# Optimization experiments

Measured on AMD Instinct MI355X. Metric: run time of the kernel, lower is better.

Reference implementation:

```python
import jax, jax.numpy as jnp
import numpy as np

B, DIM, OC, H, W, HEADS = 4, 128, 128, 128, 128, 8
L = H * W
_BN_INV = 1.0 / (1.0 + 1e-5) ** 0.5  # eval-mode BN: running_mean=0, running_var=1


def conv2d(x, w, b=None, groups=1, pad=0):
    y = jax.lax.conv_general_dilated(
        x, w, (1, 1), [(pad, pad), (pad, pad)],
        dimension_numbers=('NCHW', 'OIHW', 'NCHW'),
        feature_group_count=groups)
    if b is not None:
        y = y + b[None, :, None, None]
    return y


def bn(x, g, b):
    return x * (g * _BN_INV)[None, :, None, None] + b[None, :, None, None]


def ln(x, g, b, eps=1e-5):
    m = jnp.mean(x, -1, keepdims=True)
    v = jnp.mean((x - m) ** 2, -1, keepdims=True)
    return (x - m) * jax.lax.rsqrt(v + eps) * g + b


def rope_tables(h, w, c, base=10000.0):
    k_max = c // 4
    theta = 1.0 / base ** (np.arange(k_max, dtype=np.float32) / k_max)
    gi, gj = np.meshgrid(np.arange(h, dtype=np.float32),
                         np.arange(w, dtype=np.float32), indexing='ij')
    ang = np.concatenate([gi[..., None] * theta, gj[..., None] * theta], -1)  # (h,w,c//2)
    return jnp.asarray(np.cos(ang)), jnp.asarray(np.sin(ang))


def apply_rope(x, cs, sn):  # x: (b,h,w,c); consecutive pairs = (re, im)
    xr, xi = x[..., 0::2], x[..., 1::2]
    return jnp.stack([cs * xr - sn * xi, sn * xr + cs * xi], -1).reshape(x.shape)


def linear_attn(x, qk_w, qk_b, lepe_w, lepe_b, h, w):
    b, n, c = x.shape
    hd = c // HEADS
    qk = x @ qk_w.T + qk_b
    q = jax.nn.elu(qk[..., :c]) + 1.0
    k = jax.nn.elu(qk[..., c:]) + 1.0
    cs, sn = rope_tables(h, w, c)

    def heads(t):  # (b,n,c) -> (b,HEADS,n,hd)
        return t.reshape(b, n, HEADS, hd).transpose(0, 2, 1, 3)

    q_r = heads(apply_rope(q.reshape(b, h, w, c), cs, sn).reshape(b, n, c))
    k_r = heads(apply_rope(k.reshape(b, h, w, c), cs, sn).reshape(b, n, c))
    qh, kh, vh = heads(q), heads(k), heads(x)
    k_mean = jnp.mean(kh, axis=2, keepdims=True)                      # (b,Hd,1,hd)
    z = 1.0 / (jnp.einsum('bhnd,bhmd->bhnm', qh, k_mean) + 1e-6)      # (b,Hd,n,1)
    s = n ** -0.5
    kv = jnp.einsum('bhnd,bhne->bhde', k_r * s, vh * s)               # (b,Hd,hd,hd)
    out = jnp.einsum('bhnd,bhde->bhne', q_r, kv) * z
    out = out.transpose(0, 2, 1, 3).reshape(b, n, c)
    v_img = x.reshape(b, h, w, c).transpose(0, 3, 1, 2)
    lepe = conv2d(v_img, lepe_w, lepe_b, groups=c, pad=1)
    return out + lepe.transpose(0, 2, 3, 1).reshape(b, n, c)


def fmt_block(xb, fw1, fb1, f_g, f_be, fw2, fb2, n_g, n_be):
    t = jnp.fft.fft2(xb)                                              # (B,C,H,W) complex
    wgt = jax.nn.relu(bn(conv2d(t.real, fw1, fb1), f_g, f_be))
    wgt = jax.nn.sigmoid(conv2d(wgt, fw2, fb2))
    f = jnp.abs(jnp.fft.ifft2(wgt * t))
    f = jax.nn.relu(bn(f, n_g, n_be))
    return f.reshape(f.shape[0], f.shape[1], -1).transpose(0, 2, 1)   # (B,L,C)


def _forward(x, c1_w, c1_b, c1_g, c1_be, cpe1_w, cpe1_b,
             fw1, fb1, f_g, f_be, fw2, fb2, nbn_g, nbn_be,
             ln1_g, ln1_b, d3w1, d3b1, d3w2, d5w1, d5b1, d5w2,
             ap_w, ap_b, ip2_w, ip2_b, dwc2_w, dwc2_b,
             qk_w, qk_b, lepe_w, lepe_b, op_w, op_b,
             cpe2_w, cpe2_b, ln2_g, ln2_b,
             ffn_w1, ffn_b1, ffn_w2, ffn_b2, po_w,
             red_w, red_b, red_g, red_be):
    Bb, C, Hh, Ww = x.shape
    Ll = Hh * Ww
    to_img = lambda t: t.reshape(Bb, Hh, Ww, C).transpose(0, 3, 1, 2)   # (B,L,C)->(B,C,H,W)
    to_seq = lambda t: t.transpose(0, 2, 3, 1).reshape(Bb, Ll, -1)       # (B,C,H,W)->(B,L,C)

    x_0 = jax.nn.relu(bn(conv2d(x, c1_w, c1_b), c1_g, c1_be))           # (B,OC,H,W)
    xt = to_seq(x + conv2d(x, cpe1_w, cpe1_b, groups=C, pad=1))
    shortcut = xt
    fmt1 = fmt_block(to_img(xt), fw1, fb1, f_g, f_be, fw2, fb2, nbn_g, nbn_be)

    x_s = ln(xt, ln1_g, ln1_b)
    xs_img = to_img(x_s)
    x_s3 = conv2d(conv2d(xs_img, d3w1, d3b1), d3w2, None, groups=C // 2, pad=1)
    x_s5 = conv2d(conv2d(xs_img, d5w1, d5b1), d5w2, None, groups=C // 2, pad=2)
    act_res = jax.nn.silu(to_seq(conv2d(xs_img, ap_w, ap_b)))

    def branch(t):  # (B,C/2,H,W) -> (B,L,C/2)
        t = conv2d(t, ip2_w, ip2_b)
        t = jax.nn.silu(conv2d(t, dwc2_w, dwc2_b, groups=C // 2, pad=1))
        return to_seq(t)

    a3 = linear_attn(branch(x_s3), qk_w, qk_b, lepe_w, lepe_b, Hh, Ww)
    a5 = linear_attn(branch(x_s5), qk_w, qk_b, lepe_w, lepe_b, Hh, Ww)
    xs = jnp.concatenate([a3, a5], -1)
    xs = to_seq(conv2d(to_img(xs * act_res), op_w, op_b))

    xt = shortcut + xs + fmt1
    xt = xt + to_seq(conv2d(to_img(xt), cpe2_w, cpe2_b, groups=C, pad=1))
    fmt2 = fmt_block(to_img(xt), fw1, fb1, f_g, f_be, fw2, fb2, nbn_g, nbn_be)
    h2 = ln(xt, ln2_g, ln2_b)
    ffn = jax.nn.gelu(h2 @ ffn_w1.T + ffn_b1, approximate=False) @ ffn_w2.T + ffn_b2
    xt = xt + ffn + fmt2

    xo = conv2d(to_img(xt), po_w)                                        # (B,OC,H,W)
    cat = jnp.concatenate([x_0, xo], 1)
    return jax.nn.relu(bn(conv2d(cat, red_w, red_b), red_g, red_be)) + x_0


def setup_inputs():
    key = jax.random.key(0)
    it = iter(jax.random.split(key, 64))

    def w(shape, s=0.05):
        return jax.random.normal(next(it), shape, jnp.float32) * s

    d, oc = DIM, OC
    ones = lambda n: jnp.ones((n,), jnp.float32)
    zeros = lambda n: jnp.zeros((n,), jnp.float32)
    return {
        'x': jax.random.normal(next(it), (B, d, H, W), jnp.float32),
        'c1_w': w((oc, d, 1, 1)), 'c1_b': w((oc,), 0.01), 'c1_g': ones(oc), 'c1_be': zeros(oc),
        'cpe1_w': w((d, 1, 3, 3)), 'cpe1_b': w((d,), 0.01),
        'fw1': w((d // 16, d, 1, 1)), 'fb1': w((d // 16,), 0.01),
        'f_g': ones(d // 16), 'f_be': zeros(d // 16),
        'fw2': w((d, d // 16, 1, 1)), 'fb2': w((d,), 0.01),
        'nbn_g': ones(d), 'nbn_be': zeros(d),
        'ln1_g': ones(d), 'ln1_b': zeros(d),
        'd3w1': w((d, d, 1, 1)), 'd3b1': w((d,), 0.01), 'd3w2': w((d // 2, 2, 3, 3)),
        'd5w1': w((d, d, 1, 1)), 'd5b1': w((d,), 0.01), 'd5w2': w((d // 2, 2, 5, 5)),
        'ap_w': w((d, d, 1, 1)), 'ap_b': w((d,), 0.01),
        'ip2_w': w((d // 2, d // 2, 1, 1)), 'ip2_b': w((d // 2,), 0.01),
        'dwc2_w': w((d // 2, 1, 3, 3)), 'dwc2_b': w((d // 2,), 0.01),
        'qk_w': w((d, d // 2)), 'qk_b': w((d,), 0.01),
        'lepe_w': w((d // 2, 1, 3, 3)), 'lepe_b': w((d // 2,), 0.01),
        'op_w': w((d, d, 1, 1)), 'op_b': w((d,), 0.01),
        'cpe2_w': w((d, 1, 3, 3)), 'cpe2_b': w((d,), 0.01),
        'ln2_g': ones(d), 'ln2_b': zeros(d),
        'ffn_w1': w((4, d)), 'ffn_b1': w((4,), 0.01),
        'ffn_w2': w((d, 4)), 'ffn_b2': w((d,), 0.01),
        'po_w': w((oc, d, 1, 1)),
        'red_w': w((oc, 2 * oc, 1, 1)), 'red_b': w((oc,), 0.01),
        'red_g': ones(oc), 'red_be': zeros(oc),
    }


def reference(x, c1_w, c1_b, c1_g, c1_be, cpe1_w, cpe1_b,
              fw1, fb1, f_g, f_be, fw2, fb2, nbn_g, nbn_be,
              ln1_g, ln1_b, d3w1, d3b1, d3w2, d5w1, d5b1, d5w2,
              ap_w, ap_b, ip2_w, ip2_b, dwc2_w, dwc2_b,
              qk_w, qk_b, lepe_w, lepe_b, op_w, op_b,
              cpe2_w, cpe2_b, ln2_g, ln2_b,
              ffn_w1, ffn_b1, ffn_w2, ffn_b2, po_w,
              red_w, red_b, red_g, red_be):
    return _forward(x, c1_w, c1_b, c1_g, c1_be, cpe1_w, cpe1_b,
                    fw1, fb1, f_g, f_be, fw2, fb2, nbn_g, nbn_be,
                    ln1_g, ln1_b, d3w1, d3b1, d3w2, d5w1, d5b1, d5w2,
                    ap_w, ap_b, ip2_w, ip2_b, dwc2_w, dwc2_b,
                    qk_w, qk_b, lepe_w, lepe_b, op_w, op_b,
                    cpe2_w, cpe2_b, ln2_g, ln2_b,
                    ffn_w1, ffn_b1, ffn_w2, ffn_b2, po_w,
                    red_w, red_b, red_g, red_be)
```

## Files before the change

kernel.cpp:

```cpp
#include <hip/hip_runtime.h>
#include <math.h>

typedef unsigned short bf16_t;
typedef __attribute__((ext_vector_type(8))) short short8;
typedef __attribute__((ext_vector_type(4))) float f32x4;

#define B_ 4
#define C_ 128
#define H_ 128
#define W_ 128
#define L_ (H_*W_)
#define NS  ((size_t)B_*L_*C_)
#define NH  ((size_t)B_*L_*64)
#define NSP ((size_t)L_*C_)
#define PI_F 3.14159265358979323846f
#define BN_INV 0.9999950000374997f
#define THETA_SC 0.8304820237218406f
#define TOTW 157148
#define W16SHIFT 107548

__device__ __forceinline__ float ldf(bf16_t v){ return __uint_as_float(((unsigned)v)<<16); }
__device__ __forceinline__ bf16_t f2b(float f){
  unsigned u = __float_as_uint(f);
  u += 0x7fffu + ((u>>16)&1u);
  return (bf16_t)(u>>16);
}

#define WGSZ ((size_t)B_*8*L_)
#define ACCSZ 2304
#define CWSZ 157184
#define CW16SZF 78592
#define WSF (6*NS + 3*NH + WGSZ + ACCSZ + CWSZ + CW16SZF + 16)
__device__ float g_ws[WSF];

__global__ void k_probe(const bf16_t* __restrict__ xb, int* __restrict__ flag){
  __shared__ int vote;
  if (threadIdx.x == 0) vote = 0;
  __syncthreads();
  int bad = 0;
  for (int i = threadIdx.x; i < 2048; i += 256) {
    float v = ldf(xb[2*i]);
    if (!(fabsf(v) < 1e6f)) bad = 1;
  }
  if (bad) atomicOr(&vote, 1);
  __syncthreads();
  if (threadIdx.x == 0) *flag = vote;
}

struct P47 { const void* p[47]; };
__device__ __constant__ int c_wsz[47] = {
  16384,128,128,128,1152,128,1024,8,8,8,1024,128,128,128,128,128,
  16384,128,1152,16384,128,3200,16384,128,4096,64,576,64,8192,128,
  576,64,16384,128,1152,128,128,128,512,4,512,128,16384,32768,128,128,128};

__global__ __launch_bounds__(256) void k_cvt(P47 ps, const int* __restrict__ flagp,
                                             float* __restrict__ dst){
  int g = blockIdx.x*256 + threadIdx.x;
  if (g >= TOTW) return;
  int fl = *flagp;
  int idx = 0, off = g;
  while (off >= c_wsz[idx]) { off -= c_wsz[idx]; idx++; }
  const void* s = ps.p[idx];
  dst[g] = fl ? ((const float*)s)[off] : ldf(((const bf16_t*)s)[off]);
}

__global__ __launch_bounds__(256) void k_cvt16(const float* __restrict__ src, bf16_t* __restrict__ dst){
  int g = blockIdx.x*256 + threadIdx.x;
  if (g >= TOTW) return;
  dst[g + (g >= W16SHIFT ? 4 : 0)] = f2b(src[g]);
}

__global__ void k_zero(float* p, int n){
  int i = blockIdx.x*256 + threadIdx.x;
  if (i < n) p[i] = 0.f;
}

__device__ __forceinline__ void tw_fwd(int lane, float* tc, float* ts) {
  sincosf(-PI_F * (float)lane * (1.f/64.f), &ts[0], &tc[0]);
  int i = 1;
  #pragma unroll
  for (int m = 32; m >= 1; m >>= 1, i++) {
    int k = lane & (m-1);
    sincosf(-PI_F * (float)k / (float)m, &ts[i], &tc[i]);
  }
}
__device__ __forceinline__ void tw_inv(int lane, float* tc, float* ts) {
  int i = 0;
  #pragma unroll
  for (int m = 1; m <= 32; m <<= 1, i++) {
    int k = lane & (m-1);
    sincosf(PI_F * (float)k / (float)m, &ts[i], &tc[i]);
  }
  sincosf(PI_F * (float)lane * (1.f/64.f), &ts[6], &tc[6]);
}

__device__ __forceinline__ void fft128_fwd(float& lor, float& loi, float& hir, float& hii,
                                           int lane, const float* tc, const float* ts) {
  {
    float s = ts[0], c = tc[0];
    float ar = lor, ai = loi;
    float dr = ar - hir, di = ai - hii;
    lor = ar + hir; loi = ai + hii;
    hir = dr*c - di*s; hii = dr*s + di*c;
  }
  int i = 1;
  #pragma unroll
  for (int m = 32; m >= 1; m >>= 1, i++) {
    float s = ts[i], c = tc[i];
    bool up = (lane & m) != 0;
    {
      float orr = __shfl_xor(lor, m), oii = __shfl_xor(loi, m);
      float sr = lor + orr, si = loi + oii;
      float dr = orr - lor, di = oii - loi;
      float tr = dr*c - di*s, ti = dr*s + di*c;
      lor = up ? tr : sr; loi = up ? ti : si;
    }
    {
      float orr = __shfl_xor(hir, m), oii = __shfl_xor(hii, m);
      float sr = hir + orr, si = hii + oii;
      float dr = orr - hir, di = oii - hii;
      float tr = dr*c - di*s, ti = dr*s + di*c;
      hir = up ? tr : sr; hii = up ? ti : si;
    }
  }
}

__device__ __forceinline__ void fft128_inv(float& lor, float& loi, float& hir, float& hii,
                                           int lane, const float* tc, const float* ts) {
  int i = 0;
  #pragma unroll
  for (int m = 1; m <= 32; m <<= 1, i++) {
    float s = ts[i], c = tc[i];
    bool up = (lane & m) != 0;
    {
      float orr = __shfl_xor(lor, m), oii = __shfl_xor(loi, m);
      float qr = orr*c - oii*s, qi = orr*s + oii*c;
      float lo_r = lor + qr, lo_i = loi + qi;
      float mr = lor*c - loi*s, mi = lor*s + loi*c;
      float up_r = orr - mr, up_i = oii - mi;
      lor = up ? up_r : lo_r; loi = up ? up_i : lo_i;
    }
    {
      float orr = __shfl_xor(hir, m), oii = __shfl_xor(hii, m);
      float qr = orr*c - oii*s, qi = orr*s + oii*c;
      float lo_r = hir + qr, lo_i = hii + qi;
      float mr = hir*c - hii*s, mi = hir*s + hii*c;
      float up_r = orr - mr, up_i = oii - mi;
      hir = up ? up_r : lo_r; hii = up ? up_i : lo_i;
    }
  }
  {
    float s = ts[6], c = tc[6];
    float qr = hir*c - hii*s, qi = hir*s + hii*c;
    float pr = lor, pi = loi;
    lor = pr + qr; loi = pi + qi;
    hir = pr - qr; hii = pi - qi;
  }
}

__global__ __launch_bounds__(256) void k_fft_row_fwd_seq(
    const float* __restrict__ in, float* __restrict__ re, float* __restrict__ im) {
  __shared__ float T[64*130];
  int tid = threadIdx.x;
  int bid = blockIdx.x;
  int ch = (bid & 1) * 64;
  int h  = (bid >> 1) & 127;
  int b  = bid >> 8;
  const float* ip = in + ((size_t)b*L_ + (size_t)h*128)*128 + ch;
  #pragma unroll
  for (int it = 0; it < 8; it++) {
    int idx = it*256 + tid;
    int c4 = (idx & 15)*4, w = idx >> 4;
    float4 v = *(const float4*)(ip + (size_t)w*128 + c4);
    T[(c4+0)*130 + w] = v.x;
    T[(c4+1)*130 + w] = v.y;
    T[(c4+2)*130 + w] = v.z;
    T[(c4+3)*130 + w] = v.w;
  }
  __syncthreads();
  int lane = tid & 63, wv = tid >> 6;
  float tc[7], ts[7];
  tw_fwd(lane, tc, ts);
  size_t obase = (size_t)(b*128 + ch)*L_ + (size_t)h*128;
  for (int i = 0; i < 16; i++) {
    int cc = wv*16 + i;
    float lor = T[cc*130 + lane], loi = 0.f;
    float hir = T[cc*130 + 64 + lane], hii = 0.f;
    fft128_fwd(lor, loi, hir, hii, lane, tc, ts);
    size_t o = obase + (size_t)cc*L_;
    re[o + lane] = lor;      im[o + lane] = loi;
    re[o + lane + 64] = hir; im[o + lane + 64] = hii;
  }
}

__global__ __launch_bounds__(256) void k_fft_col_fwd(float* __restrict__ re, float* __restrict__ im) {
  __shared__ float Lre[128][33];
  __shared__ float Lim[128][33];
  int tid = threadIdx.x;
  size_t img = blockIdx.x >> 2;
  int w0 = (blockIdx.x & 3) * 32;
  float* rp = re + img * (size_t)L_ + w0;
  float* ip = im + img * (size_t)L_ + w0;
  for (int i = tid; i < 4096; i += 256) {
    int h = i >> 5, wl = i & 31;
    Lre[h][wl] = rp[(size_t)h*W_ + wl];
    Lim[h][wl] = ip[(size_t)h*W_ + wl];
  }
  __syncthreads();
  int lane = tid & 63, wv = tid >> 6;
  float tc[7], ts[7];
  tw_fwd(lane, tc, ts);
  for (int i = 0; i < 8; i++) {
    int col = wv*8 + i;
    float lor = Lre[lane][col], loi = Lim[lane][col];
    float hir = Lre[lane+64][col], hii = Lim[lane+64][col];
    fft128_fwd(lor, loi, hir, hii, lane, tc, ts);
    Lre[lane][col]=lor; Lim[lane][col]=loi;
    Lre[lane+64][col]=hir; Lim[lane+64][col]=hii;
  }
  __syncthreads();
  for (int i = tid; i < 4096; i += 256) {
    int h = i >> 5, wl = i & 31;
    rp[(size_t)h*W_ + wl] = Lre[h][wl];
    ip[(size_t)h*W_ + wl] = Lim[h][wl];
  }
}

__global__ __launch_bounds__(256) void k_fft_col_inv_scaled(
    float* __restrict__ re, float* __restrict__ im,
    const float* __restrict__ wg1, const float* __restrict__ fw2,
    const float* __restrict__ fb2) {
  __shared__ float Lre[128][33];
  __shared__ float Lim[128][33];
  __shared__ float w2r[8];
  int tid = threadIdx.x;
  size_t img = blockIdx.x >> 2;
  int c = (int)(img & 127);
  int b = (int)(img >> 7);
  int w0 = (blockIdx.x & 3) * 32;
  if (tid < 8) w2r[tid] = fw2[c*8 + tid];
  float b2 = fb2[c];
  float* rp = re + img * (size_t)L_ + w0;
  float* ip = im + img * (size_t)L_ + w0;
  const float* wgp = wg1 + (size_t)b*8*L_ + w0;
  __syncthreads();
  for (int i = tid; i < 4096; i += 256) {
    int h = i >> 5, wl = i & 31;
    size_t p = (size_t)h*W_ + wl;
    float a = b2;
    #pragma unroll
    for (int o = 0; o < 8; o++) a += w2r[o] * wgp[(size_t)o*L_ + p];
    float wgt = 1.f/(1.f+expf(-a));
    Lre[h][wl] = rp[p] * wgt;
    Lim[h][wl] = ip[p] * wgt;
  }
  __syncthreads();
  int lane = tid & 63, wv = tid >> 6;
  float tc[7], ts[7];
  tw_inv(lane, tc, ts);
  for (int i = 0; i < 8; i++) {
    int col = wv*8 + i;
    float lor = Lre[lane][col], loi = Lim[lane][col];
    float hir = Lre[lane+64][col], hii = Lim[lane+64][col];
    fft128_inv(lor, loi, hir, hii, lane, tc, ts);
    Lre[lane][col]=lor*(1.f/128.f); Lim[lane][col]=loi*(1.f/128.f);
    Lre[lane+64][col]=hir*(1.f/128.f); Lim[lane+64][col]=hii*(1.f/128.f);
  }
  __syncthreads();
  for (int i = tid; i < 4096; i += 256) {
    int h = i >> 5, wl = i & 31;
    rp[(size_t)h*W_ + wl] = Lre[h][wl];
    ip[(size_t)h*W_ + wl] = Lim[h][wl];
  }
}

__global__ __launch_bounds__(256) void k_fft_row_inv_abs_seq(
    const float* __restrict__ re, const float* __restrict__ im,
    const float* __restrict__ ng, const float* __restrict__ nbe,
    const float* __restrict__ add1, const float* __restrict__ add2,
    float* __restrict__ out) {
  __shared__ float T[64*130];
  int tid = threadIdx.x;
  int bid = blockIdx.x;
  int ch = (bid & 1) * 64;
  int h  = (bid >> 1) & 127;
  int b  = bid >> 8;
  int lane = tid & 63, wv = tid >> 6;
  float tc[7], ts[7];
  tw_inv(lane, tc, ts);
  size_t ibase = (size_t)(b*128 + ch)*L_ + (size_t)h*128;
  for (int i = 0; i < 16; i++) {
    int cc = wv*16 + i;
    size_t o = ibase + (size_t)cc*L_;
    float lor = re[o + lane], loi = im[o + lane];
    float hir = re[o + lane + 64], hii = im[o + lane + 64];
    fft128_inv(lor, loi, hir, hii, lane, tc, ts);
    float sg = ng[ch+cc]*BN_INV, sb = nbe[ch+cc];
    T[cc*130 + lane]      = fmaxf(sqrtf(lor*lor+loi*loi)*(1.f/128.f)*sg + sb, 0.f);
    T[cc*130 + 64 + lane] = fmaxf(sqrtf(hir*hir+hii*hii)*(1.f/128.f)*sg + sb, 0.f);
  }
  __syncthreads();
  size_t sb0 = ((size_t)b*L_ + (size_t)h*128)*128 + ch;
  #pragma unroll
  for (int it = 0; it < 8; it++) {
    int idx = it*256 + tid;
    int c4 = (idx & 15)*4, w = idx >> 4;
    size_t off = sb0 + (size_t)w*128 + c4;
    float4 v;
    v.x = T[(c4+0)*130 + w];
    v.y = T[(c4+1)*130 + w];
    v.z = T[(c4+2)*130 + w];
    v.w = T[(c4+3)*130 + w];
    float4 x1 = *(const float4*)(add1 + off);
    float4 x2 = *(const float4*)(add2 + off);
    v.x += x1.x + x2.x; v.y += x1.y + x2.y;
    v.z += x1.z + x2.z; v.w += x1.w + x2.w;
    *(float4*)(out + off) = v;
  }
}

__global__ __launch_bounds__(256) void k_freq1(const float* __restrict__ tre,
    const float* __restrict__ fw1, const float* __restrict__ fb1,
    const float* __restrict__ fg, const float* __restrict__ fbe,
    float* __restrict__ wg1) {
  __shared__ float w1s[1024];
  int tid = threadIdx.x;
  for (int i = tid; i < 1024; i += 256) w1s[i] = fw1[i];
  __syncthreads();
  size_t g = (size_t)blockIdx.x*256 + tid;
  int p = (int)(g & (L_-1));
  int b = (int)(g >> 14);
  const float* tp = tre + (size_t)b*128*L_ + p;
  float acc[8];
  #pragma unroll
  for (int o = 0; o < 8; o++) acc[o] = 0.f;
  for (int c = 0; c < 128; c++) {
    float v = tp[(size_t)c*L_];
    #pragma unroll
    for (int o = 0; o < 8; o++) acc[o] += w1s[o*128+c]*v;
  }
  size_t ob = (size_t)b*8*L_ + p;
  #pragma unroll
  for (int o = 0; o < 8; o++) {
    float v = (acc[o] + fb1[o]) * (fg[o]*BN_INV) + fbe[o];
    wg1[ob + (size_t)o*L_] = fmaxf(v, 0.f);
  }
}

template<bool DUAL>
__global__ void k_p2s(const void* __restrict__ src, float* __restrict__ dst,
                      const float* __restrict__ add1, const float* __restrict__ add2,
                      const int* __restrict__ flagp) {
  __shared__ float tile[32][33];
  int fl = DUAL ? *flagp : 1;
  int b = blockIdx.z;
  int p0 = blockIdx.x*32, c0 = blockIdx.y*32;
  int tx = threadIdx.x, ty = threadIdx.y;
  size_t base_in = (size_t)b*NSP;
  #pragma unroll
  for (int k = 0; k < 4; k++) {
    size_t off = base_in + (size_t)(c0+ty+8*k)*L_ + p0 + tx;
    float v;
    if (DUAL && !fl) v = ldf(((const bf16_t*)src)[off]);
    else             v = ((const float*)src)[off];
    tile[ty+8*k][tx] = v;
  }
  __syncthreads();
  size_t base = (size_t)b*NSP;
  #pragma unroll
  for (int k = 0; k < 4; k++) {
    size_t idx = base + (size_t)(p0+ty+8*k)*C_ + c0 + tx;
    float v = tile[tx][ty+8*k];
    if (add1) v += add1[idx];
    if (add2) v += add2[idx];
    dst[idx] = v;
  }
}

template<int CC, int MODE>
__global__ __launch_bounds__(256) void k_dw3(const float* __restrict__ in,
    const float* __restrict__ w, const float* __restrict__ bias,
    float* __restrict__ out) {
  __shared__ float wl[9*CC];
  int tid = threadIdx.x;
  for (int i = tid; i < 9*CC; i += 256) {
    int tap = i / CC, ch = i % CC;
    wl[i] = w[ch*9 + tap];
  }
  __syncthreads();
  size_t g = (size_t)blockIdx.x*256 + tid;
  int c = (int)(g & (CC-1));
  float wr[9];
  #pragma unroll
  for (int t = 0; t < 9; t++) wr[t] = wl[t*CC + c];
  size_t s = g / CC;
  int w0 = (int)(s & 31) * 4;
  int hp = (int)((s >> 5) & 127);
  int b  = (int)(s >> 12);
  const float* ip = in + (size_t)b*L_*CC + c;
  float bi = bias[c];
  float a0 = bi, a1 = bi, a2 = bi, a3 = bi;
  #pragma unroll
  for (int dh = -1; dh <= 1; dh++) {
    int h2 = hp + dh;
    if ((unsigned)h2 >= 128u) continue;
    const float* rp = ip + (size_t)h2*W_*CC;
    float px[6];
    #pragma unroll
    for (int x = 0; x < 6; x++) {
      int w2 = w0 - 1 + x;
      px[x] = ((unsigned)w2 < 128u) ? rp[(size_t)w2*CC] : 0.f;
    }
    #pragma unroll
    for (int dw = 0; dw < 3; dw++) {
      float f = wr[(dh+1)*3 + dw];
      a0 += f*px[dw];   a1 += f*px[dw+1];
      a2 += f*px[dw+2]; a3 += f*px[dw+3];
    }
  }
  size_t tb = (size_t)b*L_ + (size_t)hp*W_ + w0;
  if (MODE == 0) {
    out[(tb+0)*CC + c] = in[(tb+0)*CC + c] + a0;
    out[(tb+1)*CC + c] = in[(tb+1)*CC + c] + a1;
    out[(tb+2)*CC + c] = in[(tb+2)*CC + c] + a2;
    out[(tb+3)*CC + c] = in[(tb+3)*CC + c] + a3;
  } else {
    out[(tb+0)*CC + c] = a0 / (1.f + expf(-a0));
    out[(tb+1)*CC + c] = a1 / (1.f + expf(-a1));
    out[(tb+2)*CC + c] = a2 / (1.f + expf(-a2));
    out[(tb+3)*CC + c] = a3 / (1.f + expf(-a3));
  }
}

template<int K>
__global__ __launch_bounds__(256) void k_gconv(const float* __restrict__ in,
    const float* __restrict__ w, float* __restrict__ out) {
  __shared__ float wl[K*K*128];
  int tid = threadIdx.x;
  for (int i = tid; i < 128*K*K; i += 256) {
    int tap = i >> 7, ch = i & 127;
    wl[i] = w[ch*(K*K) + tap];
  }
  __syncthreads();
  size_t g = (size_t)blockIdx.x*256 + tid;
  int oc = (int)(g & 63);
  float wx[K*K], wy[K*K];
  #pragma unroll
  for (int t = 0; t < K*K; t++) {
    wx[t] = wl[t*128 + 2*oc];
    wy[t] = wl[t*128 + 2*oc + 1];
  }
  size_t s = g >> 6;
  int w0 = (int)(s & 31) * 4;
  int hp = (int)((s >> 5) & 127);
  int b  = (int)(s >> 12);
  const float* ip = in + (size_t)b*L_*128 + 2*oc;
  constexpr int P = K/2;
  float a0 = 0.f, a1 = 0.f, a2 = 0.f, a3 = 0.f;
  #pragma unroll
  for (int kh = 0; kh < K; kh++) {
    int h2 = hp + kh - P;
    if ((unsigned)h2 >= 128u) continue;
    const float* rp = ip + (size_t)h2*W_*128;
    float2 px[K+3];
    #pragma unroll
    for (int x = 0; x < K+3; x++) {
      int w2 = w0 - P + x;
      px[x] = ((unsigned)w2 < 128u) ? *(const float2*)(rp + (size_t)w2*128)
                                    : make_float2(0.f, 0.f);
    }
    #pragma unroll
    for (int kw = 0; kw < K; kw++) {
      float fx = wx[kh*K + kw], fy = wy[kh*K + kw];
      a0 += fx*px[kw+0].x + fy*px[kw+0].y;
      a1 += fx*px[kw+1].x + fy*px[kw+1].y;
      a2 += fx*px[kw+2].x + fy*px[kw+2].y;
      a3 += fx*px[kw+3].x + fy*px[kw+3].y;
    }
  }
  size_t tb = (size_t)b*L_ + (size_t)hp*W_ + w0;
  out[(tb+0)*64 + oc] = a0;
  out[(tb+1)*64 + oc] = a1;
  out[(tb+2)*64 + oc] = a2;
  out[(tb+3)*64 + oc] = a3;
}

template<int CIN, int COUT, int EPI, bool MUL>
__global__ __launch_bounds__(256) void k_mfma_tok(
    const float* __restrict__ in, const float* __restrict__ mulp,
    const bf16_t* __restrict__ W16, const float* __restrict__ bias,
    float* __restrict__ out) {
  constexpr int NO = COUT/16;
  int tid = threadIdx.x;
  int lane = tid & 63, wv = tid >> 6;
  int m = lane & 15, q = lane >> 4;
  size_t t0 = (size_t)blockIdx.x*64 + (size_t)wv*16;
  f32x4 acc[NO];
  #pragma unroll
  for (int i = 0; i < NO; i++) acc[i] = (f32x4){0.f,0.f,0.f,0.f};
  for (int k0 = 0; k0 < CIN; k0 += 32) {
    const float* ap = in + (t0 + m)*CIN + k0 + q*8;
    float4 a0 = *(const float4*)ap;
    float4 a1 = *(const float4*)(ap + 4);
    if (MUL) {
      const float* mp = mulp + (t0 + m)*CIN + k0 + q*8;
      float4 m0 = *(const float4*)mp;
      float4 m1 = *(const float4*)(mp + 4);
      a0.x*=m0.x; a0.y*=m0.y; a0.z*=m0.z; a0.w*=m0.w;
      a1.x*=m1.x; a1.y*=m1.y; a1.z*=m1.z; a1.w*=m1.w;
    }
    union { short s[8]; short8 v; } af;
    af.s[0]=(short)f2b(a0.x); af.s[1]=(short)f2b(a0.y);
    af.s[2]=(short)f2b(a0.z); af.s[3]=(short)f2b(a0.w);
    af.s[4]=(short)f2b(a1.x); af.s[5]=(short)f2b(a1.y);
    af.s[6]=(short)f2b(a1.z); af.s[7]=(short)f2b(a1.w);
    #pragma unroll
    for (int o = 0; o < NO; o++) {
      short8 bf = *(const short8*)(W16 + (size_t)(o*16 + m)*CIN + k0 + q*8);
      acc[o] = __builtin_amdgcn_mfma_f32_16x16x32_bf16(af.v, bf, acc[o], 0, 0, 0);
    }
  }
  #pragma unroll
  for (int o = 0; o < NO; o++) {
    float bv = (EPI >= 1) ? bias[o*16 + m] : 0.f;
    #pragma unroll
    for (int r = 0; r < 4; r++) {
      int row = q*4 + r;
      float v = acc[o][r] + bv;
      if (EPI == 2) v = v / (1.f + expf(-v));
      if (EPI == 3) v = v > 0.f ? v + 1.f : expf(v);
      out[(t0 + row)*COUT + o*16 + m] = v;
    }
  }
}

template<int CIN, bool DUALOUT, bool ADDX>
__global__ __launch_bounds__(256) void k_mfma_pout(
    const float* __restrict__ in1, const float* __restrict__ in2,
    const bf16_t* __restrict__ W16, const float* __restrict__ bias,
    const float* __restrict__ gam, const float* __restrict__ bet,
    const float* __restrict__ addp, void* __restrict__ out,
    const int* __restrict__ flagp) {
  constexpr int NO = 8;
  int fl = DUALOUT ? *flagp : 1;
  int tid = threadIdx.x;
  int lane = tid & 63, wv = tid >> 6;
  int m = lane & 15, q = lane >> 4;
  size_t t0 = (size_t)blockIdx.x*64 + (size_t)wv*16;
  f32x4 acc[NO];
  #pragma unroll
  for (int i = 0; i < NO; i++) acc[i] = (f32x4){0.f,0.f,0.f,0.f};
  for (int k0 = 0; k0 < CIN; k0 += 32) {
    const float* src = (CIN == 128 || k0 < 128)
        ? (in1 + (t0 + m)*128 + k0)
        : (in2 + (t0 + m)*128 + (k0 - 128));
    float4 a0 = *(const float4*)(src + q*8);
    float4 a1 = *(const float4*)(src + q*8 + 4);
    union { short s[8]; short8 v; } af;
    af.s[0]=(short)f2b(a0.x); af.s[1]=(short)f2b(a0.y);
    af.s[2]=(short)f2b(a0.z); af.s[3]=(short)f2b(a0.w);
    af.s[4]=(short)f2b(a1.x); af.s[5]=(short)f2b(a1.y);
    af.s[6]=(short)f2b(a1.z); af.s[7]=(short)f2b(a1.w);
    #pragma unroll
    for (int o = 0; o < NO; o++) {
      short8 bf = *(const short8*)(W16 + (size_t)(o*16 + m)*CIN + k0 + q*8);
      acc[o] = __builtin_amdgcn_mfma_f32_16x16x32_bf16(af.v, bf, acc[o], 0, 0, 0);
    }
  }
  int b = (int)(t0 >> 14);
  int p0 = (int)(t0 & (L_-1)) + q*4;
  #pragma unroll
  for (int ot = 0; ot < NO; ot++) {
    int o = ot*16 + m;
    float bi = bias[o], gm = gam[o]*BN_INV, be = bet[o];
    size_t idx = ((size_t)b*128 + o)*L_ + p0;
    float4 r4;
    float* rr = (float*)&r4;
    #pragma unroll
    for (int r = 0; r < 4; r++) {
      float v = acc[ot][r] + bi;
      v = fmaxf(v*gm + be, 0.f);
      rr[r] = v;
    }
    if (ADDX) {
      float4 av = *(const float4*)(addp + idx);
      r4.x += av.x; r4.y += av.y; r4.z += av.z; r4.w += av.w;
    }
    if (DUALOUT && !fl) {
      ushort4 s4;
      s4.x = f2b(r4.x); s4.y = f2b(r4.y); s4.z = f2b(r4.z); s4.w = f2b(r4.w);
      *(ushort4*)((bf16_t*)out + idx) = s4;
    } else {
      *(float4*)((float*)out + idx) = r4;
    }
  }
}

__global__ __launch_bounds__(256) void k_ln(const float* __restrict__ in,
    const float* __restrict__ g, const float* __restrict__ be, float* __restrict__ out) {
  int tid = threadIdx.x, lane = tid & 63;
  size_t t = (size_t)blockIdx.x*4 + (tid >> 6);
  const float* row = in + t*128;
  float2 v = *(const float2*)(row + lane*2);
  float s = v.x + v.y, ss = v.x*v.x + v.y*v.y;
  #pragma unroll
  for (int m = 1; m < 64; m <<= 1) { s += __shfl_xor(s, m); ss += __shfl_xor(ss, m); }
  float mean = s*(1.f/128.f);
  float inv = rsqrtf(ss*(1.f/128.f) - mean*mean + 1e-5f);
  float2 o;
  o.x = (v.x-mean)*inv*g[lane*2]   + be[lane*2];
  o.y = (v.y-mean)*inv*g[lane*2+1] + be[lane*2+1];
  *(float2*)(out + t*128 + lane*2) = o;
}

__global__ __launch_bounds__(256) void k_ln_ffn(const float* __restrict__ in,
    const float* __restrict__ g, const float* __restrict__ be,
    const float* __restrict__ w1, const float* __restrict__ b1,
    const float* __restrict__ w2, const float* __restrict__ b2,
    float* __restrict__ out) {
  int tid = threadIdx.x, lane = tid & 63;
  size_t t = (size_t)blockIdx.x*4 + (tid >> 6);
  const float* row = in + t*128;
  float2 v = *(const float2*)(row + lane*2);
  float s = v.x + v.y, ss = v.x*v.x + v.y*v.y;
  #pragma unroll
  for (int m = 1; m < 64; m <<= 1) { s += __shfl_xor(s, m); ss += __shfl_xor(ss, m); }
  float mean = s*(1.f/128.f);
  float inv = rsqrtf(ss*(1.f/128.f) - mean*mean + 1e-5f);
  float hx = (v.x-mean)*inv*g[lane*2]   + be[lane*2];
  float hy = (v.y-mean)*inv*g[lane*2+1] + be[lane*2+1];
  float hp0 = hx*w1[0*128+lane*2] + hy*w1[0*128+lane*2+1];
  float hp1 = hx*w1[1*128+lane*2] + hy*w1[1*128+lane*2+1];
  float hp2 = hx*w1[2*128+lane*2] + hy*w1[2*128+lane*2+1];
  float hp3 = hx*w1[3*128+lane*2] + hy*w1[3*128+lane*2+1];
  #pragma unroll
  for (int m = 1; m < 64; m <<= 1) {
    hp0 += __shfl_xor(hp0, m); hp1 += __shfl_xor(hp1, m);
    hp2 += __shfl_xor(hp2, m); hp3 += __shfl_xor(hp3, m);
  }
  float hv0, hv1, hv2, hv3;
  { float a = hp0 + b1[0]; hv0 = 0.5f*a*(1.f+erff(a*0.7071067811865476f)); }
  { float a = hp1 + b1[1]; hv1 = 0.5f*a*(1.f+erff(a*0.7071067811865476f)); }
  { float a = hp2 + b1[2]; hv2 = 0.5f*a*(1.f+erff(a*0.7071067811865476f)); }
  { float a = hp3 + b1[3]; hv3 = 0.5f*a*(1.f+erff(a*0.7071067811865476f)); }
  int cx = lane*2, cy = lane*2+1;
  float2 o;
  o.x = hv0*w2[cx*4+0] + hv1*w2[cx*4+1] + hv2*w2[cx*4+2] + hv3*w2[cx*4+3] + b2[cx];
  o.y = hv0*w2[cy*4+0] + hv1*w2[cy*4+1] + hv2*w2[cy*4+2] + hv3*w2[cy*4+3] + b2[cy];
  *(float2*)(out + t*128 + lane*2) = o;
}

__global__ __launch_bounds__(256) void k_kv(
    const float* __restrict__ qk, const float* __restrict__ v,
    float* __restrict__ akv_g, float* __restrict__ aks_g) {
  __shared__ float kvred[512];
  __shared__ float ksred[64];
  int tid = threadIdx.x;
  for (int i = tid; i < 512; i += 256) kvred[i] = 0.f;
  if (tid < 64) ksred[tid] = 0.f;
  __syncthreads();
  int lane = tid & 63, wv = tid >> 6;
  size_t t0 = (size_t)blockIdx.x * 64;
  int b = (int)(t0 >> 14);
  int pr = lane >> 1;
  float theta = exp2f(-(float)(pr & 15) * THETA_SC);
  bool use_i = pr < 16;
  int hbase = lane & 56;
  float akv[8];
  #pragma unroll
  for (int d = 0; d < 8; d++) akv[d] = 0.f;
  float aks = 0.f;
  for (int it = 0; it < 16; it++) {
    size_t t = t0 + (size_t)wv*16 + it;
    float k = qk[t*128 + 64 + lane];
    float xv = v[t*64 + lane];
    int l = (int)(t & (L_-1));
    float pos = use_i ? (float)(l >> 7) : (float)(l & 127);
    float sn, cs; sincosf(pos*theta, &sn, &cs);
    float kp = __shfl_xor(k, 1);
    float kr = (lane & 1) ? (sn*kp + cs*k) : (cs*k - sn*kp);
    #pragma unroll
    for (int d = 0; d < 8; d++) {
      float krd = __shfl(kr, hbase + d);
      akv[d] += krd * xv;
    }
    aks += k;
  }
  int h8 = lane >> 3, e = lane & 7;
  #pragma unroll
  for (int d = 0; d < 8; d++)
    atomicAdd(&kvred[h8*64 + d*8 + e], akv[d]);
  atomicAdd(&ksred[lane], aks);
  __syncthreads();
  for (int i = tid; i < 512; i += 256) atomicAdd(&akv_g[b*512 + i], kvred[i]);
  if (tid < 64) atomicAdd(&aks_g[b*64 + tid], ksred[tid]);
}

__global__ __launch_bounds__(256) void k_attn2(
    const float* __restrict__ qk, const float* __restrict__ x,
    const float* __restrict__ akv_g, const float* __restrict__ aks_g,
    const float* __restrict__ lw, const float* __restrict__ lb,
    float* __restrict__ out, int coff) {
  __shared__ float kv[512];
  __shared__ float km[64];
  __shared__ float lwl[576];
  int tid = threadIdx.x;
  size_t t0 = (size_t)blockIdx.x * 32;
  int b = (int)(t0 >> 14);
  const float invn = 1.f/16384.f;
  for (int i = tid; i < 512; i += 256) kv[i] = akv_g[b*512 + i]*invn;
  if (tid < 64) km[tid] = aks_g[b*64 + tid]*invn;
  for (int i = tid; i < 576; i += 256) lwl[i] = lw[i];
  __syncthreads();
  int lane = tid & 63, wv = tid >> 6;
  int pr = lane >> 1;
  float theta = exp2f(-(float)(pr & 15) * THETA_SC);
  bool use_i = pr < 16;
  int hbase = lane & 56, e = lane & 7;
  float lbv = lb[lane];
  const float* xb = x + ((size_t)b << 14) * 64;
  for (int it = 0; it < 8; it++) {
    size_t t = t0 + (size_t)wv*8 + it;
    int l = (int)(t & (L_-1));
    int ipos = l >> 7, jpos = l & 127;
    float q = qk[t*128 + lane];
    float p = q * km[lane];
    p += __shfl_xor(p, 1); p += __shfl_xor(p, 2); p += __shfl_xor(p, 4);
    float z = 1.f/(p + 1e-6f);
    float pos = use_i ? (float)ipos : (float)jpos;
    float sn, cs; sincosf(pos*theta, &sn, &cs);
    float qp = __shfl_xor(q, 1);
    float qr = (lane & 1) ? (sn*qp + cs*q) : (cs*q - sn*qp);
    float acc = 0.f;
    #pragma unroll
    for (int d = 0; d < 8; d++) {
      float qrd = __shfl(qr, hbase + d);
      acc += qrd * kv[hbase*8 + d*8 + e];
    }
    acc *= z;
    float lp = lbv;
    #pragma unroll
    for (int dh = -1; dh <= 1; dh++) {
      int h2 = ipos + dh; if ((unsigned)h2 >= 128u) continue;
      #pragma unroll
      for (int dw = -1; dw <= 1; dw++) {
        int w2 = jpos + dw; if ((unsigned)w2 >= 128u) continue;
        lp += lwl[lane*9 + (dh+1)*3 + (dw+1)] * xb[((size_t)(h2 << 7) + w2)*64 + lane];
      }
    }
    out[t*128 + coff + lane] = acc + lp;
  }
}

extern "C" void kernel_launch(void* const* d_in, const int* in_sizes, int n_in,
                              void* d_out, int out_size, void* d_ws, size_t ws_size,
                              hipStream_t stream) {
  (void)in_sizes; (void)n_in; (void)out_size;

  float* base;
  if (ws_size >= WSF * sizeof(float)) {
    base = (float*)d_ws;
  } else {
    void* p = nullptr;
    hipGetSymbolAddress(&p, HIP_SYMBOL(g_ws));
    base = (float*)p;
  }
  float* P0 = base;
  float* PA = base + 1*NS;
  float* PB = base + 2*NS;
  float* PC = base + 3*NS;
  float* PD = base + 4*NS;
  float* PF = base + 5*NS;
  float* H0 = base + 6*NS;
  float* H1 = H0 + NH;
  float* H2 = H1 + NH;
  float* WG = H2 + NH;
  float* ACC = WG + WGSZ;
  float* CW  = ACC + ACCSZ;
  bf16_t* CW16 = (bf16_t*)(CW + CWSZ);
  int*   FLG = (int*)(CW + CWSZ + CW16SZF);

  static const int wsz[47] = {
    16384,128,128,128,1152,128,1024,8,8,8,1024,128,128,128,128,128,
    16384,128,1152,16384,128,3200,16384,128,4096,64,576,64,8192,128,
    576,64,16384,128,1152,128,128,128,512,4,512,128,16384,32768,128,128,128};
  int woff[47]; { int a = 0; for (int i = 0; i < 47; i++){ woff[i] = a; a += wsz[i]; } }
  const float* Wf[47]; for (int i = 0; i < 47; i++) Wf[i] = CW + woff[i];
  auto W16 = [&](int i){ return (const bf16_t*)(CW16 + woff[i] + (woff[i] >= W16SHIFT ? 4 : 0)); };
  const float *c1_b=Wf[1], *c1_g=Wf[2], *c1_be=Wf[3], *cpe1_w=Wf[4],
    *cpe1_b=Wf[5], *fw1=Wf[6], *fb1=Wf[7], *f_g=Wf[8], *f_be=Wf[9], *fw2=Wf[10],
    *fb2=Wf[11], *nbn_g=Wf[12], *nbn_be=Wf[13], *ln1_g=Wf[14], *ln1_b=Wf[15],
    *d3b1=Wf[17], *d3w2=Wf[18], *d5b1=Wf[20],
    *d5w2=Wf[21], *ap_b=Wf[23], *ip2_b=Wf[25],
    *dwc2_w=Wf[26], *dwc2_b=Wf[27], *qk_b=Wf[29], *lepe_w=Wf[30],
    *lepe_b=Wf[31], *op_b=Wf[33], *cpe2_w=Wf[34], *cpe2_b=Wf[35],
    *ln2_g=Wf[36], *ln2_b=Wf[37], *ffn_w1=Wf[38], *ffn_b1=Wf[39], *ffn_w2=Wf[40],
    *ffn_b2=Wf[41], *red_b=Wf[44], *red_g=Wf[45], *red_be=Wf[46];
  const bf16_t *c1_w16=W16(0), *d3w1_16=W16(16), *d5w1_16=W16(19), *ap_w16=W16(22),
    *ip2_w16=W16(24), *qk_w16=W16(28), *op_w16=W16(32), *po_w16=W16(42), *red_w16=W16(43);

  const void* x = d_in[0];

  k_probe<<<1, 256, 0, stream>>>((const bf16_t*)x, FLG);
  P47 ps; for (int i = 0; i < 47; i++) ps.p[i] = d_in[i+1];
  k_cvt<<<(TOTW+255)/256, 256, 0, stream>>>(ps, FLG, CW);
  k_cvt16<<<(TOTW+255)/256, 256, 0, stream>>>(CW, CW16);

  dim3 tgrid(512, 4, 4), tblk(32, 8);

  auto fmt_fused = [&](const float* seq_in, float* re, float* im,
                       const float* add1, const float* add2, float* outp) {
    k_fft_row_fwd_seq<<<1024, 256, 0, stream>>>(seq_in, re, im);
    k_fft_col_fwd<<<2048, 256, 0, stream>>>(re, im);
    k_freq1<<<256, 256, 0, stream>>>(re, fw1, fb1, f_g, f_be, WG);
    k_fft_col_inv_scaled<<<2048, 256, 0, stream>>>(re, im, WG, fw2, fb2);
    k_fft_row_inv_abs_seq<<<1024, 256, 0, stream>>>(re, im, nbn_g, nbn_be, add1, add2, outp);
  };

  auto attn = [&](const float* brin, float* qkbuf, int coff) {
    k_zero<<<9, 256, 0, stream>>>(ACC, 2304);
    k_mfma_tok<64,128,3,false><<<1024, 256, 0, stream>>>(brin, nullptr, qk_w16, qk_b, qkbuf);
    k_kv<<<1024, 256, 0, stream>>>(qkbuf, brin, ACC, ACC + B_*512);
    k_attn2<<<2048, 256, 0, stream>>>(qkbuf, brin, ACC, ACC + B_*512, lepe_w, lepe_b, PF, coff);
  };

  k_p2s<true><<<tgrid, tblk, 0, stream>>>(x, PA, nullptr, nullptr, FLG);
  k_mfma_pout<128,false,false><<<1024, 256, 0, stream>>>(
      PA, nullptr, c1_w16, c1_b, c1_g, c1_be, nullptr, P0, FLG);
  k_dw3<128,0><<<8192, 256, 0, stream>>>(PA, cpe1_w, cpe1_b, PB);
  k_ln<<<16384, 256, 0, stream>>>(PB, ln1_g, ln1_b, PA);
  k_mfma_tok<128,128,1,false><<<1024, 256, 0, stream>>>(PA, nullptr, d3w1_16, d3b1, PD);
  k_gconv<3><<<4096, 256, 0, stream>>>(PD, d3w2, H0);
  k_mfma_tok<128,128,1,false><<<1024, 256, 0, stream>>>(PA, nullptr, d5w1_16, d5b1, PD);
  k_gconv<5><<<4096, 256, 0, stream>>>(PD, d5w2, H1);
  k_mfma_tok<128,128,2,false><<<1024, 256, 0, stream>>>(PA, nullptr, ap_w16, ap_b, PA);
  k_mfma_tok<64,64,1,false><<<1024, 256, 0, stream>>>(H0, nullptr, ip2_w16, ip2_b, H2);
  k_dw3<64,1><<<4096, 256, 0, stream>>>(H2, dwc2_w, dwc2_b, H0);
  attn(H0, PD, 0);
  k_mfma_tok<64,64,1,false><<<1024, 256, 0, stream>>>(H1, nullptr, ip2_w16, ip2_b, H2);
  k_dw3<64,1><<<4096, 256, 0, stream>>>(H2, dwc2_w, dwc2_b, H1);
  attn(H1, PD, 64);
  k_mfma_tok<128,128,1,true><<<1024, 256, 0, stream>>>(PF, PA, op_w16, op_b, PF);
  fmt_fused(PB, PC, PD, PB, PF, PB);
  k_dw3<128,0><<<8192, 256, 0, stream>>>(PB, cpe2_w, cpe2_b, PC);
  k_ln_ffn<<<16384, 256, 0, stream>>>(PC, ln2_g, ln2_b, ffn_w1, ffn_b1, ffn_w2, ffn_b2, PF);
  fmt_fused(PC, PB, PD, PC, PF, PC);
  k_mfma_tok<128,128,0,false><<<1024, 256, 0, stream>>>(PC, nullptr, po_w16, nullptr, PD);
  k_p2s<false><<<tgrid, tblk, 0, stream>>>(P0, PB, nullptr, nullptr, nullptr);
  k_mfma_pout<256,true,true><<<1024, 256, 0, stream>>>(
      PB, PD, red_w16, red_b, red_g, red_be, P0, d_out, FLG);
}
```

Measured before the change: 1.017 ms.

## Keep conv1 output token-major and transpose final output via shared memory

```diff
diff --git a/kernel.cpp b/kernel.cpp
--- a/kernel.cpp
+++ b/kernel.cpp
@@ -534,15 +534,11 @@
   }
 }
 
-template<int CIN, bool DUALOUT, bool ADDX>
-__global__ __launch_bounds__(256) void k_mfma_pout(
-    const float* __restrict__ in1, const float* __restrict__ in2,
-    const bf16_t* __restrict__ W16, const float* __restrict__ bias,
-    const float* __restrict__ gam, const float* __restrict__ bet,
-    const float* __restrict__ addp, void* __restrict__ out,
-    const int* __restrict__ flagp) {
+__global__ __launch_bounds__(256) void k_mfma_c1(
+    const float* __restrict__ in, const bf16_t* __restrict__ W16,
+    const float* __restrict__ bias, const float* __restrict__ gam,
+    const float* __restrict__ bet, float* __restrict__ out) {
   constexpr int NO = 8;
-  int fl = DUALOUT ? *flagp : 1;
   int tid = threadIdx.x;
   int lane = tid & 63, wv = tid >> 6;
   int m = lane & 15, q = lane >> 4;
@@ -550,10 +546,53 @@
   f32x4 acc[NO];
   #pragma unroll
   for (int i = 0; i < NO; i++) acc[i] = (f32x4){0.f,0.f,0.f,0.f};
-  for (int k0 = 0; k0 < CIN; k0 += 32) {
-    const float* src = (CIN == 128 || k0 < 128)
-        ? (in1 + (t0 + m)*128 + k0)
-        : (in2 + (t0 + m)*128 + (k0 - 128));
+  for (int k0 = 0; k0 < 128; k0 += 32) {
+    const float* ap = in + (t0 + m)*128 + k0 + q*8;
+    float4 a0 = *(const float4*)ap;
+    float4 a1 = *(const float4*)(ap + 4);
+    union { short s[8]; short8 v; } af;
+    af.s[0]=(short)f2b(a0.x); af.s[1]=(short)f2b(a0.y);
+    af.s[2]=(short)f2b(a0.z); af.s[3]=(short)f2b(a0.w);
+    af.s[4]=(short)f2b(a1.x); af.s[5]=(short)f2b(a1.y);
+    af.s[6]=(short)f2b(a1.z); af.s[7]=(short)f2b(a1.w);
+    #pragma unroll
+    for (int o = 0; o < NO; o++) {
+      short8 bf = *(const short8*)(W16 + (size_t)(o*16 + m)*128 + k0 + q*8);
+      acc[o] = __builtin_amdgcn_mfma_f32_16x16x32_bf16(af.v, bf, acc[o], 0, 0, 0);
+    }
+  }
+  #pragma unroll
+  for (int o = 0; o < NO; o++) {
+    int oc = o*16 + m;
+    float bi = bias[oc], gm = gam[oc]*BN_INV, be = bet[oc];
+    #pragma unroll
+    for (int r = 0; r < 4; r++) {
+      int row = q*4 + r;
+      float v = acc[o][r] + bi;
+      out[(t0 + row)*128 + oc] = fmaxf(v*gm + be, 0.f);
+    }
+  }
+}
+
+__global__ __launch_bounds__(256) void k_mfma_red(
+    const float* __restrict__ x0s, const float* __restrict__ xo,
+    const bf16_t* __restrict__ W16, const float* __restrict__ bias,
+    const float* __restrict__ gam, const float* __restrict__ bet,
+    void* __restrict__ out, const int* __restrict__ flagp) {
+  __shared__ float T[128*65];
+  constexpr int NO = 8;
+  int fl = *flagp;
+  int tid = threadIdx.x;
+  int lane = tid & 63, wv = tid >> 6;
+  int m = lane & 15, q = lane >> 4;
+  size_t t0 = (size_t)blockIdx.x*64;
+  size_t tw = t0 + (size_t)wv*16;
+  f32x4 acc[NO];
+  #pragma unroll
+  for (int i = 0; i < NO; i++) acc[i] = (f32x4){0.f,0.f,0.f,0.f};
+  for (int k0 = 0; k0 < 256; k0 += 32) {
+    const float* src = (k0 < 128) ? (x0s + (tw + m)*128 + k0)
+                                  : (xo  + (tw + m)*128 + (k0 - 128));
     float4 a0 = *(const float4*)(src + q*8);
     float4 a1 = *(const float4*)(src + q*8 + 4);
     union { short s[8]; short8 v; } af;
@@ -563,35 +602,37 @@
     af.s[6]=(short)f2b(a1.z); af.s[7]=(short)f2b(a1.w);
     #pragma unroll
     for (int o = 0; o < NO; o++) {
-      short8 bf = *(const short8*)(W16 + (size_t)(o*16 + m)*CIN + k0 + q*8);
+      short8 bf = *(const short8*)(W16 + (size_t)(o*16 + m)*256 + k0 + q*8);
       acc[o] = __builtin_amdgcn_mfma_f32_16x16x32_bf16(af.v, bf, acc[o], 0, 0, 0);
     }
   }
-  int b = (int)(t0 >> 14);
-  int p0 = (int)(t0 & (L_-1)) + q*4;
   #pragma unroll
   for (int ot = 0; ot < NO; ot++) {
     int o = ot*16 + m;
     float bi = bias[o], gm = gam[o]*BN_INV, be = bet[o];
-    size_t idx = ((size_t)b*128 + o)*L_ + p0;
-    float4 r4;
-    float* rr = (float*)&r4;
     #pragma unroll
     for (int r = 0; r < 4; r++) {
+      int row = q*4 + r;
       float v = acc[ot][r] + bi;
       v = fmaxf(v*gm + be, 0.f);
-      rr[r] = v;
-    }
-    if (ADDX) {
-      float4 av = *(const float4*)(addp + idx);
-      r4.x += av.x; r4.y += av.y; r4.z += av.z; r4.w += av.w;
-    }
-    if (DUALOUT && !fl) {
-      ushort4 s4;
-      s4.x = f2b(r4.x); s4.y = f2b(r4.y); s4.z = f2b(r4.z); s4.w = f2b(r4.w);
-      *(ushort4*)((bf16_t*)out + idx) = s4;
-    } else {
-      *(float4*)((float*)out + idx) = r4;
+      v += x0s[(tw + row)*128 + o];
+      T[o*65 + wv*16 + row] = v;
+    }
+  }
+  __syncthreads();
+  int b = (int)(t0 >> 14);
+  int p0 = (int)(t0 & (L_-1));
+  if (!fl) {
+    bf16_t* op = (bf16_t*)out;
+    for (int i = tid; i < 8192; i += 256) {
+      int o = i >> 6, tk = i & 63;
+      op[((size_t)b*128 + o)*L_ + p0 + tk] = f2b(T[o*65 + tk]);
+    }
+  } else {
+    float* op = (float*)out;
+    for (int i = tid; i < 8192; i += 256) {
+      int o = i >> 6, tk = i & 63;
+      op[((size_t)b*128 + o)*L_ + p0 + tk] = T[o*65 + tk];
     }
   }
 }
@@ -825,8 +866,7 @@
   };
 
   k_p2s<true><<<tgrid, tblk, 0, stream>>>(x, PA, nullptr, nullptr, FLG);
-  k_mfma_pout<128,false,false><<<1024, 256, 0, stream>>>(
-      PA, nullptr, c1_w16, c1_b, c1_g, c1_be, nullptr, P0, FLG);
+  k_mfma_c1<<<1024, 256, 0, stream>>>(PA, c1_w16, c1_b, c1_g, c1_be, P0);
   k_dw3<128,0><<<8192, 256, 0, stream>>>(PA, cpe1_w, cpe1_b, PB);
   k_ln<<<16384, 256, 0, stream>>>(PB, ln1_g, ln1_b, PA);
   k_mfma_tok<128,128,1,false><<<1024, 256, 0, stream>>>(PA, nullptr, d3w1_16, d3b1, PD);
@@ -846,7 +886,5 @@
   k_ln_ffn<<<16384, 256, 0, stream>>>(PC, ln2_g, ln2_b, ffn_w1, ffn_b1, ffn_w2, ffn_b2, PF);
   fmt_fused(PC, PB, PD, PC, PF, PC);
   k_mfma_tok<128,128,0,false><<<1024, 256, 0, stream>>>(PC, nullptr, po_w16, nullptr, PD);
-  k_p2s<false><<<tgrid, tblk, 0, stream>>>(P0, PB, nullptr, nullptr, nullptr);
-  k_mfma_pout<256,true,true><<<1024, 256, 0, stream>>>(
-      PB, PD, red_w16, red_b, red_g, red_be, P0, d_out, FLG);
-}
+  k_mfma_red<<<1024, 256, 0, stream>>>(P0, PD, red_w16, red_b, red_g, red_be, d_out, FLG);
+}
```

Measured after the change: 1.003 ms. About the same (-1.4%).
